# Kernel tuning notes

Hardware: AMD Instinct MI355X
Metric: run time of the kernel (lower is better)

## Reference

```python
import jax, jax.numpy as jnp
import numpy as np


def _hsig(x):
    return jnp.clip(x + 3.0, 0.0, 6.0) / 6.0


def _conv3x3(x, w, b):
    y = jax.lax.conv_general_dilated(x, w, (1, 1), ((1, 1), (1, 1)),
                                     dimension_numbers=('NCHW', 'OIHW', 'NCHW'))
    return y + b[None, :, None, None]


def _group_norm(x, gamma, beta, groups=16, eps=1e-5):
    B, C, H, W = x.shape
    xg = x.reshape(B, groups, C // groups, H, W)
    mu = xg.mean(axis=(2, 3, 4), keepdims=True)
    var = ((xg - mu) ** 2).mean(axis=(2, 3, 4), keepdims=True)
    xn = ((xg - mu) * jax.lax.rsqrt(var + eps)).reshape(B, C, H, W)
    return xn * gamma[None, :, None, None] + beta[None, :, None, None]


def _resize_bilinear(x, Ho, Wo):
    # bilinear, align_corners=True, NCHW
    B, C, H, W = x.shape
    if (H, W) == (Ho, Wo):
        return x
    ys = jnp.linspace(0.0, H - 1.0, Ho)
    xs = jnp.linspace(0.0, W - 1.0, Wo)
    y0 = jnp.floor(ys).astype(jnp.int32); y1 = jnp.minimum(y0 + 1, H - 1)
    x0 = jnp.floor(xs).astype(jnp.int32); x1 = jnp.minimum(x0 + 1, W - 1)
    wy = (ys - y0)[None, None, :, None]
    wx = (xs - x0)[None, None, None, :]
    rows = x[:, :, y0, :] * (1 - wy) + x[:, :, y1, :] * wy  # [B,C,Ho,W]
    return rows[:, :, :, x0] * (1 - wx) + rows[:, :, :, x1] * wx


def _bilinear_sample(img, py, px):
    # img: [C,H,W]; py/px: [K2,Ho,Wo] float coords; zero padding outside
    C, H, W = img.shape
    flat = img.reshape(C, -1)
    y0 = jnp.floor(py); x0 = jnp.floor(px)
    wy = py - y0; wx = px - x0

    def corner(yi, xi, w):
        valid = (yi >= 0) & (yi <= H - 1) & (xi >= 0) & (xi <= W - 1)
        idx = (jnp.clip(yi.astype(jnp.int32), 0, H - 1) * W
               + jnp.clip(xi.astype(jnp.int32), 0, W - 1))
        v = flat[:, idx.reshape(-1)].reshape((C,) + idx.shape)
        return v * (w * valid)[None]

    return (corner(y0, x0, (1 - wy) * (1 - wx))
            + corner(y0, x0 + 1, (1 - wy) * wx)
            + corner(y0 + 1, x0, wy * (1 - wx))
            + corner(y0 + 1, x0 + 1, wy * wx))


def _deform_conv(x, offset, mask, weight, stride):
    # torchvision deform_conv2d semantics, kernel 3x3, padding 1, no bias
    B, Ci, H, W = x.shape
    Co = weight.shape[0]
    K, K2 = 3, 9
    Ho, Wo = offset.shape[-2:]
    ky, kx = jnp.meshgrid(jnp.arange(K), jnp.arange(K), indexing='ij')
    base_y = (jnp.arange(Ho) * stride - 1)[None, :, None] + ky.reshape(K2, 1, 1)  # [K2,Ho,1]
    base_x = (jnp.arange(Wo) * stride - 1)[None, None, :] + kx.reshape(K2, 1, 1)  # [K2,1,Wo]
    off = offset.reshape(B, K2, 2, Ho, Wo)  # (dy, dx) per kernel tap
    py = base_y[None].astype(x.dtype) + off[:, :, 0]  # [B,K2,Ho,Wo]
    px = base_x[None].astype(x.dtype) + off[:, :, 1]
    sampled = jax.vmap(_bilinear_sample)(x, py, px)  # [B,Ci,K2,Ho,Wo]
    sampled = sampled * mask[:, None]
    return jnp.einsum('oik,bikhw->bohw', weight.reshape(Co, Ci, K2), sampled)


def _scale_attn(feat, w, b):
    pooled = feat.mean(axis=(2, 3))          # [B,C]
    s = _hsig(jax.nn.relu(pooled @ w.T + b))  # [B,1]
    return s[:, :, None, None]


def _dyrelu(x, w1, b1, w2, b2):
    pooled = x.mean(axis=(2, 3))              # [B,C]
    h = jax.nn.relu(pooled @ w1.T + b1)       # [B,C/4]
    coef = _hsig(h @ w2.T + b2) - 0.5         # [B,4C]
    a1, bb1, a2, bb2 = jnp.split(coef, 4, axis=1)
    a1 = a1 * 2.0 + 1.0
    a2 = a2 * 2.0
    e = lambda t: t[:, :, None, None]
    return jnp.maximum(x * e(a1) + e(bb1), x * e(a2) + e(bb2))


def _dyhead_forward(x0, x1, x2, w_off, b_off, w_mid, g_mid, bt_mid,
                    w_low, g_low, bt_low, w_high, g_high, bt_high,
                    w_scale, b_scale, w1, b1, w2, b2):
    xs = [x0, x1, x2]
    outs = []
    for lvl in range(3):
        om = _conv3x3(xs[lvl], w_off, b_off)
        offset = om[:, :18]
        mask = jax.nn.sigmoid(om[:, 18:])
        mid = _group_norm(_deform_conv(xs[lvl], offset, mask, w_mid, 1), g_mid, bt_mid)
        sum_feat = mid * _scale_attn(mid, w_scale, b_scale)
        n = 1.0
        if lvl > 0:
            # low level: stride-2 DCN; its output grid equals current level -> offsets reused as-is
            low = _group_norm(_deform_conv(xs[lvl - 1], offset, mask, w_low, 2), g_low, bt_low)
            sum_feat = sum_feat + low * _scale_attn(low, w_scale, b_scale)
            n += 1.0
        if lvl < 2:
            hi_in = xs[lvl + 1]
            Ht, Wt = hi_in.shape[-2], hi_in.shape[-1]
            ho = _resize_bilinear(offset, Ht, Wt)
            hm = _resize_bilinear(mask, Ht, Wt)
            hi = _group_norm(_deform_conv(hi_in, ho, hm, w_high, 1), g_high, bt_high)
            hi = _resize_bilinear(hi, xs[lvl].shape[-2], xs[lvl].shape[-1])
            sum_feat = sum_feat + hi * _scale_attn(hi, w_scale, b_scale)
            n += 1.0
        outs.append(_dyrelu(sum_feat / n, w1, b1, w2, b2))
    return tuple(outs)


def setup_inputs() -> dict:
    key = jax.random.key(0)
    ks = jax.random.split(key, 12)
    B, C = 2, 256
    x0 = jax.random.normal(ks[0], (B, C, 64, 64), jnp.float32)
    x1 = jax.random.normal(ks[1], (B, C, 32, 32), jnp.float32)
    x2 = jax.random.normal(ks[2], (B, C, 16, 16), jnp.float32)
    w_off = 0.01 * jax.random.normal(ks[3], (27, C, 3, 3), jnp.float32)
    b_off = 0.01 * jax.random.normal(ks[4], (27,), jnp.float32)
    s = 1.0 / np.sqrt(C * 9).astype(np.float32)
    w_mid = s * jax.random.normal(ks[5], (C, C, 3, 3), jnp.float32)
    w_low = s * jax.random.normal(ks[6], (C, C, 3, 3), jnp.float32)
    w_high = s * jax.random.normal(ks[7], (C, C, 3, 3), jnp.float32)
    g_mid = jnp.ones((C,), jnp.float32); bt_mid = jnp.zeros((C,), jnp.float32)
    g_low = jnp.ones((C,), jnp.float32); bt_low = jnp.zeros((C,), jnp.float32)
    g_high = jnp.ones((C,), jnp.float32); bt_high = jnp.zeros((C,), jnp.float32)
    w_scale = 0.01 * jax.random.normal(ks[8], (1, C), jnp.float32)
    b_scale = jnp.zeros((1,), jnp.float32)
    w1 = (1.0 / np.sqrt(C)) * jax.random.normal(ks[9], (C // 4, C), jnp.float32)
    b1 = jnp.zeros((C // 4,), jnp.float32)
    w2 = (1.0 / np.sqrt(C // 4)) * jax.random.normal(ks[10], (4 * C, C // 4), jnp.float32)
    b2 = jnp.zeros((4 * C,), jnp.float32)
    return dict(x0=x0, x1=x1, x2=x2, w_off=w_off, b_off=b_off,
                w_mid=w_mid, g_mid=g_mid, bt_mid=bt_mid,
                w_low=w_low, g_low=g_low, bt_low=bt_low,
                w_high=w_high, g_high=g_high, bt_high=bt_high,
                w_scale=w_scale, b_scale=b_scale, w1=w1, b1=b1, w2=w2, b2=b2)


def reference(x0, x1, x2, w_off, b_off, w_mid, g_mid, bt_mid,
              w_low, g_low, bt_low, w_high, g_high, bt_high,
              w_scale, b_scale, w1, b1, w2, b2):
    return _dyhead_forward(x0, x1, x2, w_off, b_off, w_mid, g_mid, bt_mid,
                           w_low, g_low, bt_low, w_high, g_high, bt_high,
                           w_scale, b_scale, w1, b1, w2, b2)
```

## Files before the change

kernel.cpp:

```cpp
#include <hip/hip_runtime.h>
#include <math.h>


#define NB 2
#define NC 256

typedef __attribute__((ext_vector_type(8))) short bf16x8;
typedef __attribute__((ext_vector_type(4))) float f32x4;

static __device__ __forceinline__ float hsig_(float x){
  return fminf(fmaxf(x + 3.f, 0.f), 6.f) * (1.f/6.f);
}

static __device__ __forceinline__ unsigned short bf16r(float f){
  unsigned int u = __float_as_uint(f);
  unsigned int r = (u + 0x7FFFu + ((u >> 16) & 1u)) >> 16;
  return (unsigned short)r;
}

static __device__ __forceinline__ float bf2f(unsigned short u){
  return __uint_as_float(((unsigned int)u) << 16);
}

static __device__ __forceinline__ float blk_reduce(float v, float* buf){
  int t = threadIdx.x;
  buf[t] = v; __syncthreads();
  for(int s=128; s>0; s>>=1){
    if (t < s) buf[t] += buf[t+s];
    __syncthreads();
  }
  float r = buf[0];
  __syncthreads();
  return r;
}

__global__ __launch_bounds__(256) void zero_kernel(float* __restrict__ p, int n){
  int i = blockIdx.x*256 + threadIdx.x;
  if (i < n) p[i] = 0.f;
}

__global__ __launch_bounds__(256) void xpose_kernel(
    const float* __restrict__ x, unsigned short* __restrict__ xt, int N){
  __shared__ float tile[32][65];
  int t = threadIdx.x;
  int nb = N >> 6;
  int hw0 = (blockIdx.x % nb) * 64;
  int cg8 = (blockIdx.x / nb) & 7;
  int b   = blockIdx.x / (nb*8);
  int ci0 = cg8 * 32;
  const float* xb = x + ((size_t)(b*NC + ci0))*N;
  #pragma unroll
  for (int it = 0; it < 8; ++it){
    int idx = it*256 + t;
    int ci = idx >> 6, hwl = idx & 63;
    tile[ci][hwl] = xb[(size_t)ci*N + hw0 + hwl];
  }
  __syncthreads();
  int hwl = t >> 2, cg = t & 3;
  unsigned int ou[4];
  #pragma unroll
  for (int p = 0; p < 4; ++p){
    unsigned int lo = bf16r(tile[cg*8 + 2*p][hwl]);
    unsigned int hi = bf16r(tile[cg*8 + 2*p + 1][hwl]);
    ou[p] = lo | (hi << 16);
  }
  *(uint4*)(xt + ((size_t)b*N + hw0 + hwl)*256 + ci0 + cg*8) =
      make_uint4(ou[0], ou[1], ou[2], ou[3]);
}

__global__ __launch_bounds__(256) void conv_off_tiled(
    const float* __restrict__ x, const float* __restrict__ w,
    float* __restrict__ partial, int H, int W, int tilesx){
  __shared__ float hl[18][20];
  __shared__ float wl[32][9][28];
  int b = blockIdx.z, chunk = blockIdx.y;
  int ty0 = (blockIdx.x / tilesx) * 16, tx0 = (blockIdx.x % tilesx) * 16;
  int t = threadIdx.x;
  int ci0 = chunk * 32;
  int N = H * W;
  for (int s = t; s < 27*32*9; s += 256){
    int c = s / 288, rem = s % 288, ci = rem / 9, k = rem % 9;
    wl[ci][k][c] = w[((size_t)(c*NC + ci0 + ci))*9 + k];
  }
  float acc[27];
  #pragma unroll
  for (int c = 0; c < 27; ++c) acc[c] = 0.f;
  int ty = t >> 4, tx = t & 15;
  for (int ci = 0; ci < 32; ++ci){
    const float* xc = x + ((size_t)(b*NC + ci0 + ci))*N;
    __syncthreads();
    for (int s = t; s < 324; s += 256){
      int hy = s / 18, hx = s % 18;
      int gy = ty0 + hy - 1, gx = tx0 + hx - 1;
      hl[hy][hx] = (gy >= 0 && gy < H && gx >= 0 && gx < W) ? xc[gy*W + gx] : 0.f;
    }
    __syncthreads();
    float xv[9];
    #pragma unroll
    for (int ky = 0; ky < 3; ++ky)
      #pragma unroll
      for (int kx = 0; kx < 3; ++kx)
        xv[ky*3+kx] = hl[ty+ky][tx+kx];
    #pragma unroll
    for (int k = 0; k < 9; ++k){
      float xk = xv[k];
      #pragma unroll
      for (int c4 = 0; c4 < 6; ++c4){
        float4 wv = *(float4*)&wl[ci][k][c4*4];
        acc[c4*4+0] = fmaf(wv.x, xk, acc[c4*4+0]);
        acc[c4*4+1] = fmaf(wv.y, xk, acc[c4*4+1]);
        acc[c4*4+2] = fmaf(wv.z, xk, acc[c4*4+2]);
        acc[c4*4+3] = fmaf(wv.w, xk, acc[c4*4+3]);
      }
      acc[24] = fmaf(wl[ci][k][24], xk, acc[24]);
      acc[25] = fmaf(wl[ci][k][25], xk, acc[25]);
      acc[26] = fmaf(wl[ci][k][26], xk, acc[26]);
    }
  }
  int hw = (ty0 + ty)*W + (tx0 + tx);
  float* pp = partial + ((size_t)(chunk*NB + b)*27)*N + hw;
  #pragma unroll
  for (int c = 0; c < 27; ++c) pp[(size_t)c*N] = acc[c];
}

__global__ __launch_bounds__(256) void conv_reduce(
    const float* __restrict__ partial, const float* __restrict__ bias,
    float* __restrict__ off, float* __restrict__ mask, int N){
  int idx = blockIdx.x*256 + threadIdx.x;
  int total = NB*27*N;
  if (idx >= total) return;
  int hw = idx % N;
  int c  = (idx / N) % 27;
  int b  = idx / (27*N);
  float s = bias[c];
  #pragma unroll
  for (int p = 0; p < 8; ++p)
    s += partial[((size_t)(p*NB + b)*27 + c)*N + hw];
  if (c < 18) off[((size_t)b*18 + c)*N + hw] = s;
  else        mask[((size_t)b*9 + (c-18))*N + hw] = 1.f/(1.f + expf(-s));
}

__global__ __launch_bounds__(256) void resize_pool_kernel(
    const float* __restrict__ in, float* __restrict__ out,
    float* __restrict__ pooled, int C, int H, int W, int Ho, int Wo){
  __shared__ float buf[256];
  int No = Ho*Wo;
  int idx = blockIdx.x*256 + threadIdx.x;
  int total = NB*C*No;
  float v = 0.f;
  int bc = 0;
  if (idx < total){
    int xo = idx % Wo;
    int yo = (idx / Wo) % Ho;
    bc = idx / No;
    float fy = (float)(H-1) / (float)(Ho-1);
    float fx = (float)(W-1) / (float)(Wo-1);
    float ys = yo * fy, xs = xo * fx;
    int y0 = (int)floorf(ys), x0i = (int)floorf(xs);
    int y1 = min(y0+1, H-1), x1 = min(x0i+1, W-1);
    float wy = ys - (float)y0, wx = xs - (float)x0i;
    const float* p = in + (size_t)bc*H*W;
    float v00 = p[y0*W+x0i], v01 = p[y0*W+x1];
    float v10 = p[y1*W+x0i], v11 = p[y1*W+x1];
    float r0 = v00*(1.f-wy) + v10*wy;
    float r1 = v01*(1.f-wy) + v11*wy;
    v = r0*(1.f-wx) + r1*wx;
    out[idx] = v;
  }
  if (pooled){
    float s = blk_reduce(v, buf);
    if (threadIdx.x == 0) atomicAdd(&pooled[bc], s);
  }
}

__global__ __launch_bounds__(256) void sample_t2_kernel(
    const unsigned short* __restrict__ xt, const float* __restrict__ off,
    const float* __restrict__ mask, unsigned short* __restrict__ cols,
    int Hi, int Wi, int Ho, int Wo, int stride){
  int N = Ho*Wo;
  int t = threadIdx.x;
  int c8 = t & 31, hw_l = t >> 5;
  int nb = N >> 3;
  int b  = blockIdx.x / nb;
  int hw = (blockIdx.x % nb)*8 + hw_l;
  int yo = hw / Wo, xo = hw % Wo;
  int HiWi = Hi*Wi;
  const unsigned short* xb = xt + (size_t)b*HiWi*256 + c8*8;
  const float* ob = off + (size_t)b*18*N;
  const float* mb = mask + (size_t)b*9*N;
  unsigned short* cb = cols + (size_t)b*9*N*256;
  float Hm1 = (float)(Hi-1), Wm1 = (float)(Wi-1);
  #pragma unroll
  for (int kp = 0; kp < 9; ++kp){
    int ky = kp/3, kx = kp%3;
    float py = (float)(yo*stride - 1 + ky) + ob[(size_t)(2*kp)*N + hw];
    float px = (float)(xo*stride - 1 + kx) + ob[(size_t)(2*kp+1)*N + hw];
    float m  = mb[(size_t)kp*N + hw];
    float y0f = floorf(py), x0f = floorf(px);
    float wy = py - y0f, wx = px - x0f;
    bool vy0 = (y0f >= 0.f)     && (y0f <= Hm1);
    bool vy1 = (y0f+1.f >= 0.f) && (y0f+1.f <= Hm1);
    bool vx0 = (x0f >= 0.f)     && (x0f <= Wm1);
    bool vx1 = (x0f+1.f >= 0.f) && (x0f+1.f <= Wm1);
    int y0i = min(max((int)y0f, 0), Hi-1);
    int y1i = min(max((int)y0f + 1, 0), Hi-1);
    int x0i = min(max((int)x0f, 0), Wi-1);
    int x1i = min(max((int)x0f + 1, 0), Wi-1);
    float w00 = (1.f-wy)*(1.f-wx) * (vy0 && vx0 ? 1.f : 0.f);
    float w01 = (1.f-wy)*wx       * (vy0 && vx1 ? 1.f : 0.f);
    float w10 = wy*(1.f-wx)       * (vy1 && vx0 ? 1.f : 0.f);
    float w11 = wy*wx             * (vy1 && vx1 ? 1.f : 0.f);
    const bf16x8 c00 = *(const bf16x8*)(xb + (size_t)(y0i*Wi + x0i)*256);
    const bf16x8 c01 = *(const bf16x8*)(xb + (size_t)(y0i*Wi + x1i)*256);
    const bf16x8 c10 = *(const bf16x8*)(xb + (size_t)(y1i*Wi + x0i)*256);
    const bf16x8 c11 = *(const bf16x8*)(xb + (size_t)(y1i*Wi + x1i)*256);
    unsigned int ou[4];
    #pragma unroll
    for (int p = 0; p < 4; ++p){
      float v0 = (w00*bf2f((unsigned short)c00[2*p])   + w01*bf2f((unsigned short)c01[2*p]) +
                  w10*bf2f((unsigned short)c10[2*p])   + w11*bf2f((unsigned short)c11[2*p])) * m;
      float v1 = (w00*bf2f((unsigned short)c00[2*p+1]) + w01*bf2f((unsigned short)c01[2*p+1]) +
                  w10*bf2f((unsigned short)c10[2*p+1]) + w11*bf2f((unsigned short)c11[2*p+1])) * m;
      ou[p] = (unsigned int)bf16r(v0) | ((unsigned int)bf16r(v1) << 16);
    }
    *(uint4*)(cb + ((size_t)kp*N + hw)*256 + c8*8) =
        make_uint4(ou[0], ou[1], ou[2], ou[3]);
  }
}

__global__ __launch_bounds__(256) void wtrans_t_kernel(
    const float* __restrict__ w, unsigned short* __restrict__ At){
  int j = blockIdx.x*256 + threadIdx.x;
  if (j >= 2304*256) return;
  int e = j & 7, co = (j >> 3) & 255, chunk = j >> 11;
  int kp = chunk >> 5, ci = (chunk & 31)*8 + e;
  At[j] = bf16r(w[((size_t)(co*NC + ci))*9 + kp]);
}

__global__ __launch_bounds__(256, 2) void gemm_t2_kernel(
    const unsigned short* __restrict__ At,
    const unsigned short* __restrict__ cols,
    float* __restrict__ C, float* __restrict__ stats, int N){
  int b = blockIdx.z;
  int tid = threadIdx.x;
  int wv = tid >> 6, l = tid & 63;
  int wc = wv & 1, wh = wv >> 1;
  int co0 = blockIdx.y*64 + wc*32;
  int hw0 = blockIdx.x*64 + wh*32;
  int lr = l & 15, lg = l >> 4;
  const unsigned short* Bb = cols + (size_t)b*9*N*256;
  f32x4 acc[2][2];
  #pragma unroll
  for (int mi = 0; mi < 2; ++mi)
    #pragma unroll
    for (int ni = 0; ni < 2; ++ni)
      acc[mi][ni] = (f32x4){0.f, 0.f, 0.f, 0.f};

  #define A_OFF(cidx, mi) (((size_t)(cidx)*256 + co0 + (mi)*16 + lr)*8)
  #define B_OFF(cidx, ni) (((size_t)((cidx) >> 5)*N + hw0 + (ni)*16 + lr)*256 + ((cidx) & 31)*8)

  int c0 = lg;
  bf16x8 a0 = *(const bf16x8*)(At + A_OFF(c0, 0));
  bf16x8 a1 = *(const bf16x8*)(At + A_OFF(c0, 1));
  bf16x8 b0 = *(const bf16x8*)(Bb + B_OFF(c0, 0));
  bf16x8 b1 = *(const bf16x8*)(Bb + B_OFF(c0, 1));
  for (int kc = 0; kc < 284; kc += 4){
    int cn = kc + 4 + lg;
    bf16x8 na0 = *(const bf16x8*)(At + A_OFF(cn, 0));
    bf16x8 na1 = *(const bf16x8*)(At + A_OFF(cn, 1));
    bf16x8 nb0 = *(const bf16x8*)(Bb + B_OFF(cn, 0));
    bf16x8 nb1 = *(const bf16x8*)(Bb + B_OFF(cn, 1));
    acc[0][0] = __builtin_amdgcn_mfma_f32_16x16x32_bf16(a0, b0, acc[0][0], 0, 0, 0);
    acc[0][1] = __builtin_amdgcn_mfma_f32_16x16x32_bf16(a0, b1, acc[0][1], 0, 0, 0);
    acc[1][0] = __builtin_amdgcn_mfma_f32_16x16x32_bf16(a1, b0, acc[1][0], 0, 0, 0);
    acc[1][1] = __builtin_amdgcn_mfma_f32_16x16x32_bf16(a1, b1, acc[1][1], 0, 0, 0);
    a0 = na0; a1 = na1; b0 = nb0; b1 = nb1;
  }
  acc[0][0] = __builtin_amdgcn_mfma_f32_16x16x32_bf16(a0, b0, acc[0][0], 0, 0, 0);
  acc[0][1] = __builtin_amdgcn_mfma_f32_16x16x32_bf16(a0, b1, acc[0][1], 0, 0, 0);
  acc[1][0] = __builtin_amdgcn_mfma_f32_16x16x32_bf16(a1, b0, acc[1][0], 0, 0, 0);
  acc[1][1] = __builtin_amdgcn_mfma_f32_16x16x32_bf16(a1, b1, acc[1][1], 0, 0, 0);
  #undef A_OFF
  #undef B_OFF

  #pragma unroll
  for (int mi = 0; mi < 2; ++mi){
    float s = 0.f, ss = 0.f;
    #pragma unroll
    for (int ni = 0; ni < 2; ++ni)
      #pragma unroll
      for (int r = 0; r < 4; ++r){
        float v = acc[mi][ni][r];
        int row = co0 + mi*16 + lg*4 + r;
        int col = hw0 + ni*16 + lr;
        C[((size_t)b*NC + row)*N + col] = v;
        s += v; ss = fmaf(v, v, ss);
      }
    #pragma unroll
    for (int o = 32; o > 0; o >>= 1){
      s  += __shfl_xor(s,  o);
      ss += __shfl_xor(ss, o);
    }
    if (l == 0){
      int g = b*16 + ((co0 >> 4) + mi);
      atomicAdd(&stats[g*2],     s);
      atomicAdd(&stats[g*2 + 1], ss);
    }
  }
}

__global__ __launch_bounds__(256) void gn_apply_pool(
    float* __restrict__ f, const float* __restrict__ gamma,
    const float* __restrict__ beta, const float* __restrict__ stats,
    float* __restrict__ pooled, int N, float inv_cnt){
  __shared__ float buf[256];
  int idx = blockIdx.x*256 + threadIdx.x;
  int c = (idx / N) & (NC-1);
  int b = idx / (NC*N);
  int g = b*16 + (c >> 4);
  float s_  = stats[g*2];
  float ss_ = stats[g*2 + 1];
  float mu  = s_ * inv_cnt;
  float var = ss_ * inv_cnt - mu*mu;
  float rstd = rsqrtf(var + 1e-5f);
  float v = (f[idx] - mu)*rstd*gamma[c] + beta[c];
  f[idx] = v;
  if (pooled){
    float bs = blk_reduce(v, buf);
    if (threadIdx.x == 0) atomicAdd(&pooled[b*NC + c], bs);
  }
}

__global__ __launch_bounds__(256) void attn_kernel(
    const float* __restrict__ pooled, const float* __restrict__ wsc,
    const float* __restrict__ bsc, float* __restrict__ scal, float inv_N){
  __shared__ float buf[256];
  int b = blockIdx.x;
  float v = pooled[b*NC + threadIdx.x] * inv_N * wsc[threadIdx.x];
  float t = blk_reduce(v, buf);
  if (threadIdx.x == 0){
    float z = fmaxf(t + bsc[0], 0.f);
    scal[b] = hsig_(z);
  }
}

__global__ __launch_bounds__(256) void combine_pool_kernel(
    const float* __restrict__ fm, const float* __restrict__ fl,
    const float* __restrict__ fh, const float* __restrict__ scal,
    float* __restrict__ outp, float* __restrict__ plsum,
    int N, float inv_n){
  __shared__ float buf[256];
  int idx = blockIdx.x*256 + threadIdx.x;
  int b = idx / (NC*N);
  int c = (idx / N) & (NC-1);
  float v = fm[idx] * scal[b];
  if (fl) v = fmaf(fl[idx], scal[2+b], v);
  if (fh) v = fmaf(fh[idx], scal[4+b], v);
  v *= inv_n;
  outp[idx] = v;
  float bs = blk_reduce(v, buf);
  if (threadIdx.x == 0) atomicAdd(&plsum[b*NC + c], bs);
}

__global__ __launch_bounds__(256) void dyrelu_mlp_kernel(
    const float* __restrict__ plsum,
    const float* __restrict__ w1, const float* __restrict__ b1,
    const float* __restrict__ w2, const float* __restrict__ b2,
    float* __restrict__ coef, float inv_N){
  __shared__ float pld[256];
  __shared__ float h[64];
  int b = blockIdx.x, t = threadIdx.x;
  pld[t] = plsum[b*NC + t] * inv_N;
  __syncthreads();
  if (t < 64){
    float a = b1[t];
    for(int c=0; c<256; ++c) a = fmaf(w1[t*256 + c], pld[c], a);
    h[t] = fmaxf(a, 0.f);
  }
  __syncthreads();
  for(int q=0; q<4; ++q){
    int o = q*256 + t;
    float a = b2[o];
    #pragma unroll 8
    for(int k=0; k<64; ++k) a = fmaf(w2[o*64 + k], h[k], a);
    coef[b*1024 + o] = hsig_(a) - 0.5f;
  }
}

__global__ __launch_bounds__(256) void dyrelu_apply_kernel(
    const float* __restrict__ sf, const float* __restrict__ coef,
    float* __restrict__ out, int N){
  int idx = blockIdx.x*256 + threadIdx.x;
  int c = (idx / N) & (NC-1);
  int b = idx / (NC*N);
  const float* cf = coef + b*1024;
  float a1 = fmaf(cf[c], 2.f, 1.f);
  float bb1 = cf[256 + c];
  float a2 = cf[512 + c]*2.f;
  float bb2 = cf[768 + c];
  float v = sf[idx];
  out[idx] = fmaxf(fmaf(v, a1, bb1), fmaf(v, a2, bb2));
}

extern "C" void kernel_launch(void* const* d_in, const int* in_sizes, int n_in,
                              void* d_out, int out_size, void* d_ws, size_t ws_size,
                              hipStream_t stream){
  const float* x0      = (const float*)d_in[0];
  const float* x1      = (const float*)d_in[1];
  const float* x2      = (const float*)d_in[2];
  const float* w_off   = (const float*)d_in[3];
  const float* b_off   = (const float*)d_in[4];
  const float* w_mid   = (const float*)d_in[5];
  const float* g_mid   = (const float*)d_in[6];
  const float* bt_mid  = (const float*)d_in[7];
  const float* w_low   = (const float*)d_in[8];
  const float* g_low   = (const float*)d_in[9];
  const float* bt_low  = (const float*)d_in[10];
  const float* w_high  = (const float*)d_in[11];
  const float* g_high  = (const float*)d_in[12];
  const float* bt_high = (const float*)d_in[13];
  const float* w_scale = (const float*)d_in[14];
  const float* b_scale = (const float*)d_in[15];
  const float* w1      = (const float*)d_in[16];
  const float* b1      = (const float*)d_in[17];
  const float* w2      = (const float*)d_in[18];
  const float* b2      = (const float*)d_in[19];
  float* out = (float*)d_out;

  char* wp_ = (char*)d_ws;
  auto alloc = [&](size_t bytes) -> char* {
    char* r = wp_;
    wp_ += (bytes + 255) & ~(size_t)255;
    return r;
  };
  float* off0  = (float*)alloc((size_t)NB*18*4096*4);
  float* off1  = (float*)alloc((size_t)NB*18*1024*4);
  float* off2  = (float*)alloc((size_t)NB*18*256*4);
  float* mask0 = (float*)alloc((size_t)NB*9*4096*4);
  float* mask1 = (float*)alloc((size_t)NB*9*1024*4);
  float* mask2 = (float*)alloc((size_t)NB*9*256*4);
  float* offr  = (float*)alloc((size_t)NB*18*1024*4);
  float* maskr = (float*)alloc((size_t)NB*9*1024*4);
  float* partial = (float*)alloc((size_t)8*NB*27*4096*4);
  unsigned short* Atm = (unsigned short*)alloc((size_t)2304*256*2);
  unsigned short* Atl = (unsigned short*)alloc((size_t)2304*256*2);
  unsigned short* Ath = (unsigned short*)alloc((size_t)2304*256*2);
  unsigned short* xt0 = (unsigned short*)alloc((size_t)NB*4096*256*2);
  unsigned short* xt1 = (unsigned short*)alloc((size_t)NB*1024*256*2);
  unsigned short* xt2 = (unsigned short*)alloc((size_t)NB*256*256*2);
  unsigned short* colsT = (unsigned short*)alloc((size_t)NB*9*4096*256*2);
  float* fmid  = (float*)alloc((size_t)NB*NC*4096*4);
  float* flow  = (float*)alloc((size_t)NB*NC*4096*4);
  float* fhis  = (float*)alloc((size_t)NB*NC*1024*4);
  float* fhi   = (float*)alloc((size_t)NB*NC*4096*4);
  float* sumf  = (float*)alloc((size_t)NB*NC*4096*4);
  float* statsm = (float*)alloc((size_t)(64*3 + 512*4)*4);
  float* statsl = statsm + 64;
  float* statsh = statsm + 128;
  float* plmid  = statsm + 192;
  float* pllow  = plmid + 512;
  float* plhi   = plmid + 1024;
  float* plsum  = plmid + 1536;
  const int ZN = 64*3 + 512*4;
  float* scal  = (float*)alloc(8*4);
  float* coef  = (float*)alloc((size_t)NB*1024*4);
  (void)ws_size; (void)in_sizes; (void)n_in; (void)out_size;

  wtrans_t_kernel<<<2304, 256, 0, stream>>>(w_mid, Atm);
  wtrans_t_kernel<<<2304, 256, 0, stream>>>(w_low, Atl);
  wtrans_t_kernel<<<2304, 256, 0, stream>>>(w_high, Ath);
  xpose_kernel<<<NB*8*(4096/64), 256, 0, stream>>>(x0, xt0, 4096);
  xpose_kernel<<<NB*8*(1024/64), 256, 0, stream>>>(x1, xt1, 1024);
  xpose_kernel<<<NB*8*(256/64),  256, 0, stream>>>(x2, xt2, 256);

  const int   sizes[3] = {64, 32, 16};
  const float* xs[3]   = {x0, x1, x2};
  const unsigned short* xts[3] = {xt0, xt1, xt2};
  float* OFF[3]  = {off0, off1, off2};
  float* MASK[3] = {mask0, mask1, mask2};
  const size_t outoff[3] = {0, (size_t)NB*NC*4096, (size_t)NB*NC*4096 + (size_t)NB*NC*1024};

  for(int l=0; l<3; ++l){
    int H = sizes[l], W = H, N = H*W;
    int totBCN = NB*NC*N;
    int tilesx = H/16;
    float invN = 1.f/(float)N;
    float inv_cnt = 1.f/(float)(16*N);

    zero_kernel<<<(ZN+255)/256, 256, 0, stream>>>(statsm, ZN);

    conv_off_tiled<<<dim3(tilesx*tilesx, 8, NB), 256, 0, stream>>>(
        xs[l], w_off, partial, H, W, tilesx);
    conv_reduce<<<(NB*27*N+255)/256, 256, 0, stream>>>(
        partial, b_off, OFF[l], MASK[l], N);

    sample_t2_kernel<<<NB*(N/8), 256, 0, stream>>>(
        xts[l], OFF[l], MASK[l], colsT, H, W, H, W, 1);
    gemm_t2_kernel<<<dim3(N/64, 4, NB), 256, 0, stream>>>(Atm, colsT, fmid, statsm, N);
    gn_apply_pool<<<totBCN/256, 256, 0, stream>>>(fmid, g_mid, bt_mid, statsm, plmid, N, inv_cnt);
    attn_kernel<<<NB, 256, 0, stream>>>(plmid, w_scale, b_scale, scal + 0, invN);

    int nf = 1;
    const float* flowp = nullptr;
    const float* fhip  = nullptr;

    if (l > 0){
      int Hp = sizes[l-1];
      sample_t2_kernel<<<NB*(N/8), 256, 0, stream>>>(
          xts[l-1], OFF[l], MASK[l], colsT, Hp, Hp, H, W, 2);
      gemm_t2_kernel<<<dim3(N/64, 4, NB), 256, 0, stream>>>(Atl, colsT, flow, statsl, N);
      gn_apply_pool<<<totBCN/256, 256, 0, stream>>>(flow, g_low, bt_low, statsl, pllow, N, inv_cnt);
      attn_kernel<<<NB, 256, 0, stream>>>(pllow, w_scale, b_scale, scal + 2, invN);
      nf++; flowp = flow;
    }

    if (l < 2){
      int Ht = sizes[l+1], Nt = Ht*Ht;
      float inv_cnt_h = 1.f/(float)(16*Nt);
      resize_pool_kernel<<<(NB*18*Nt+255)/256, 256, 0, stream>>>(OFF[l], offr, nullptr, 18, H, W, Ht, Ht);
      resize_pool_kernel<<<(NB*9*Nt+255)/256, 256, 0, stream>>>(MASK[l], maskr, nullptr, 9, H, W, Ht, Ht);
      sample_t2_kernel<<<NB*(Nt/8), 256, 0, stream>>>(
          xts[l+1], offr, maskr, colsT, Ht, Ht, Ht, Ht, 1);
      gemm_t2_kernel<<<dim3(Nt/64, 4, NB), 256, 0, stream>>>(Ath, colsT, fhis, statsh, Nt);
      gn_apply_pool<<<(NB*NC*Nt)/256, 256, 0, stream>>>(fhis, g_high, bt_high, statsh, nullptr, Nt, inv_cnt_h);
      resize_pool_kernel<<<totBCN/256, 256, 0, stream>>>(fhis, fhi, plhi, NC, Ht, Ht, H, W);
      attn_kernel<<<NB, 256, 0, stream>>>(plhi, w_scale, b_scale, scal + 4, invN);
      nf++; fhip = fhi;
    }

    combine_pool_kernel<<<totBCN/256, 256, 0, stream>>>(
        fmid, flowp, fhip, scal, sumf, plsum, N, 1.f/(float)nf);
    dyrelu_mlp_kernel<<<NB, 256, 0, stream>>>(plsum, w1, b1, w2, b2, coef, invN);
    dyrelu_apply_kernel<<<totBCN/256, 256, 0, stream>>>(
        sumf, coef, out + outoff[l], N);
  }
}
```

Baseline: 827.8 us.

## Split-K deformable-conv GEMM with larger per-wave tiles and atomic accumulation

The GEMM changes from 32x32 per-wave tiles over the full K=2304 to 64x64 per-wave tiles with K split into 4 chunks of 576, one chunk per blockIdx.y. Partial results are accumulated into a zeroed output buffer with float atomicAdd. The GroupNorm statistics fusion is removed and replaced by a separate stats_kernel pass, and extra zero_kernel launches are added. The aim is more register reuse per loaded fragment, at the cost of atomic traffic, an extra full read pass for stats, the zeroing passes, and losing the software prefetch of the next K step.

```diff
diff --git a/kernel.cpp b/kernel.cpp
--- a/kernel.cpp
+++ b/kernel.cpp
@@ -237,75 +237,66 @@
   At[j] = bf16r(w[((size_t)(co*NC + ci))*9 + kp]);
 }
 
-__global__ __launch_bounds__(256, 2) void gemm_t2_kernel(
+__global__ __launch_bounds__(256) void gemm_t3_kernel(
     const unsigned short* __restrict__ At,
     const unsigned short* __restrict__ cols,
-    float* __restrict__ C, float* __restrict__ stats, int N){
+    float* __restrict__ C, int N){
   int b = blockIdx.z;
+  int ks = blockIdx.y;
+  int hw0 = blockIdx.x * 64;
   int tid = threadIdx.x;
   int wv = tid >> 6, l = tid & 63;
-  int wc = wv & 1, wh = wv >> 1;
-  int co0 = blockIdx.y*64 + wc*32;
-  int hw0 = blockIdx.x*64 + wh*32;
+  int co0 = wv * 64;
   int lr = l & 15, lg = l >> 4;
   const unsigned short* Bb = cols + (size_t)b*9*N*256;
-  f32x4 acc[2][2];
-  #pragma unroll
-  for (int mi = 0; mi < 2; ++mi)
-    #pragma unroll
-    for (int ni = 0; ni < 2; ++ni)
+  f32x4 acc[4][4];
+  #pragma unroll
+  for (int mi = 0; mi < 4; ++mi)
+    #pragma unroll
+    for (int ni = 0; ni < 4; ++ni)
       acc[mi][ni] = (f32x4){0.f, 0.f, 0.f, 0.f};
-
-  #define A_OFF(cidx, mi) (((size_t)(cidx)*256 + co0 + (mi)*16 + lr)*8)
-  #define B_OFF(cidx, ni) (((size_t)((cidx) >> 5)*N + hw0 + (ni)*16 + lr)*256 + ((cidx) & 31)*8)
-
-  int c0 = lg;
-  bf16x8 a0 = *(const bf16x8*)(At + A_OFF(c0, 0));
-  bf16x8 a1 = *(const bf16x8*)(At + A_OFF(c0, 1));
-  bf16x8 b0 = *(const bf16x8*)(Bb + B_OFF(c0, 0));
-  bf16x8 b1 = *(const bf16x8*)(Bb + B_OFF(c0, 1));
-  for (int kc = 0; kc < 284; kc += 4){
-    int cn = kc + 4 + lg;
-    bf16x8 na0 = *(const bf16x8*)(At + A_OFF(cn, 0));
-    bf16x8 na1 = *(const bf16x8*)(At + A_OFF(cn, 1));
-    bf16x8 nb0 = *(const bf16x8*)(Bb + B_OFF(cn, 0));
-    bf16x8 nb1 = *(const bf16x8*)(Bb + B_OFF(cn, 1));
-    acc[0][0] = __builtin_amdgcn_mfma_f32_16x16x32_bf16(a0, b0, acc[0][0], 0, 0, 0);
-    acc[0][1] = __builtin_amdgcn_mfma_f32_16x16x32_bf16(a0, b1, acc[0][1], 0, 0, 0);
-    acc[1][0] = __builtin_amdgcn_mfma_f32_16x16x32_bf16(a1, b0, acc[1][0], 0, 0, 0);
-    acc[1][1] = __builtin_amdgcn_mfma_f32_16x16x32_bf16(a1, b1, acc[1][1], 0, 0, 0);
-    a0 = na0; a1 = na1; b0 = nb0; b1 = nb1;
-  }
-  acc[0][0] = __builtin_amdgcn_mfma_f32_16x16x32_bf16(a0, b0, acc[0][0], 0, 0, 0);
-  acc[0][1] = __builtin_amdgcn_mfma_f32_16x16x32_bf16(a0, b1, acc[0][1], 0, 0, 0);
-  acc[1][0] = __builtin_amdgcn_mfma_f32_16x16x32_bf16(a1, b0, acc[1][0], 0, 0, 0);
-  acc[1][1] = __builtin_amdgcn_mfma_f32_16x16x32_bf16(a1, b1, acc[1][1], 0, 0, 0);
-  #undef A_OFF
-  #undef B_OFF
-
-  #pragma unroll
-  for (int mi = 0; mi < 2; ++mi){
-    float s = 0.f, ss = 0.f;
-    #pragma unroll
-    for (int ni = 0; ni < 2; ++ni)
+  int base = ks * 72;
+  for (int kc = 0; kc < 72; kc += 4){
+    int cidx = base + kc + lg;
+    bf16x8 a[4], bv[4];
+    #pragma unroll
+    for (int mi = 0; mi < 4; ++mi)
+      a[mi] = *(const bf16x8*)(At + ((size_t)cidx*256 + co0 + mi*16 + lr)*8);
+    #pragma unroll
+    for (int ni = 0; ni < 4; ++ni)
+      bv[ni] = *(const bf16x8*)(Bb + ((size_t)(cidx >> 5)*N + hw0 + ni*16 + lr)*256 + (cidx & 31)*8);
+    #pragma unroll
+    for (int mi = 0; mi < 4; ++mi)
+      #pragma unroll
+      for (int ni = 0; ni < 4; ++ni)
+        acc[mi][ni] = __builtin_amdgcn_mfma_f32_16x16x32_bf16(a[mi], bv[ni], acc[mi][ni], 0, 0, 0);
+  }
+  #pragma unroll
+  for (int mi = 0; mi < 4; ++mi)
+    #pragma unroll
+    for (int ni = 0; ni < 4; ++ni)
       #pragma unroll
       for (int r = 0; r < 4; ++r){
-        float v = acc[mi][ni][r];
         int row = co0 + mi*16 + lg*4 + r;
         int col = hw0 + ni*16 + lr;
-        C[((size_t)b*NC + row)*N + col] = v;
-        s += v; ss = fmaf(v, v, ss);
+        atomicAdd(&C[((size_t)b*NC + row)*N + col], acc[mi][ni][r]);
       }
-    #pragma unroll
-    for (int o = 32; o > 0; o >>= 1){
-      s  += __shfl_xor(s,  o);
-      ss += __shfl_xor(ss, o);
-    }
-    if (l == 0){
-      int g = b*16 + ((co0 >> 4) + mi);
-      atomicAdd(&stats[g*2],     s);
-      atomicAdd(&stats[g*2 + 1], ss);
-    }
+}
+
+__global__ __launch_bounds__(256) void stats_kernel(
+    const float* __restrict__ f, float* __restrict__ stats, int N){
+  __shared__ float b1[256];
+  __shared__ float b2[256];
+  int idx = blockIdx.x*256 + threadIdx.x;
+  int c = (idx / N) & (NC-1);
+  int b = idx / (NC*N);
+  float v = f[idx];
+  float s  = blk_reduce(v, b1);
+  float ss = blk_reduce(v*v, b2);
+  if (threadIdx.x == 0){
+    int g = b*16 + (c >> 4);
+    atomicAdd(&stats[g*2],     s);
+    atomicAdd(&stats[g*2 + 1], ss);
   }
 }
 
@@ -494,9 +485,11 @@
     conv_reduce<<<(NB*27*N+255)/256, 256, 0, stream>>>(
         partial, b_off, OFF[l], MASK[l], N);
 
+    zero_kernel<<<totBCN/256, 256, 0, stream>>>(fmid, totBCN);
     sample_t2_kernel<<<NB*(N/8), 256, 0, stream>>>(
         xts[l], OFF[l], MASK[l], colsT, H, W, H, W, 1);
-    gemm_t2_kernel<<<dim3(N/64, 4, NB), 256, 0, stream>>>(Atm, colsT, fmid, statsm, N);
+    gemm_t3_kernel<<<dim3(N/64, 4, NB), 256, 0, stream>>>(Atm, colsT, fmid, N);
+    stats_kernel<<<totBCN/256, 256, 0, stream>>>(fmid, statsm, N);
     gn_apply_pool<<<totBCN/256, 256, 0, stream>>>(fmid, g_mid, bt_mid, statsm, plmid, N, inv_cnt);
     attn_kernel<<<NB, 256, 0, stream>>>(plmid, w_scale, b_scale, scal + 0, invN);
 
@@ -506,9 +499,11 @@
 
     if (l > 0){
       int Hp = sizes[l-1];
+      zero_kernel<<<totBCN/256, 256, 0, stream>>>(flow, totBCN);
       sample_t2_kernel<<<NB*(N/8), 256, 0, stream>>>(
           xts[l-1], OFF[l], MASK[l], colsT, Hp, Hp, H, W, 2);
-      gemm_t2_kernel<<<dim3(N/64, 4, NB), 256, 0, stream>>>(Atl, colsT, flow, statsl, N);
+      gemm_t3_kernel<<<dim3(N/64, 4, NB), 256, 0, stream>>>(Atl, colsT, flow, N);
+      stats_kernel<<<totBCN/256, 256, 0, stream>>>(flow, statsl, N);
       gn_apply_pool<<<totBCN/256, 256, 0, stream>>>(flow, g_low, bt_low, statsl, pllow, N, inv_cnt);
       attn_kernel<<<NB, 256, 0, stream>>>(pllow, w_scale, b_scale, scal + 2, invN);
       nf++; flowp = flow;
@@ -516,13 +511,16 @@
 
     if (l < 2){
       int Ht = sizes[l+1], Nt = Ht*Ht;
+      int totH = NB*NC*Nt;
       float inv_cnt_h = 1.f/(float)(16*Nt);
       resize_pool_kernel<<<(NB*18*Nt+255)/256, 256, 0, stream>>>(OFF[l], offr, nullptr, 18, H, W, Ht, Ht);
       resize_pool_kernel<<<(NB*9*Nt+255)/256, 256, 0, stream>>>(MASK[l], maskr, nullptr, 9, H, W, Ht, Ht);
+      zero_kernel<<<totH/256, 256, 0, stream>>>(fhis, totH);
       sample_t2_kernel<<<NB*(Nt/8), 256, 0, stream>>>(
           xts[l+1], offr, maskr, colsT, Ht, Ht, Ht, Ht, 1);
-      gemm_t2_kernel<<<dim3(Nt/64, 4, NB), 256, 0, stream>>>(Ath, colsT, fhis, statsh, Nt);
-      gn_apply_pool<<<(NB*NC*Nt)/256, 256, 0, stream>>>(fhis, g_high, bt_high, statsh, nullptr, Nt, inv_cnt_h);
+      gemm_t3_kernel<<<dim3(Nt/64, 4, NB), 256, 0, stream>>>(Ath, colsT, fhis, Nt);
+      stats_kernel<<<totH/256, 256, 0, stream>>>(fhis, statsh, Nt);
+      gn_apply_pool<<<totH/256, 256, 0, stream>>>(fhis, g_high, bt_high, statsh, nullptr, Nt, inv_cnt_h);
       resize_pool_kernel<<<totBCN/256, 256, 0, stream>>>(fhis, fhi, plhi, NC, Ht, Ht, H, W);
       attn_kernel<<<NB, 256, 0, stream>>>(plhi, w_scale, b_scale, scal + 4, invN);
       nf++; fhip = fhi;
```

After: 985.1 us. 1.19x slower.
